# Optimization experiments

Measured on AMD Instinct MI355X. Metric: run time of the kernel, lower is better.

## Reference

```python
import jax, jax.numpy as jnp
import numpy as np

SMALL = 1e-7
EPS = 1e-6


def setup_inputs() -> dict:
    key = jax.random.key(0)
    k1, k2 = jax.random.split(key)
    B, C, h, w = 8, 3, 1024, 1024
    src = jax.random.normal(k1, (B, C, h, w), dtype=jnp.float32)
    # near-identity homographies so warped coords land mostly in-bounds
    H = jnp.eye(3, dtype=jnp.float32)[None] + 0.05 * jax.random.normal(k2, (B, 3, 3), dtype=jnp.float32)
    return {"src": src, "H": H}


def reference(src, H):
    B, C, h, w = src.shape
    # homogeneous pixel grid: (3, h, w) = [x, y, 1]
    xx = jnp.arange(w, dtype=jnp.float32)
    yy = jnp.arange(h, dtype=jnp.float32)
    gx, gy = jnp.meshgrid(xx, yy)  # (h, w) each
    grid = jnp.stack([gx, gy, jnp.ones_like(gx)], axis=0)  # (3, h, w)

    # per-pixel homography transform: (B,3,h,w)
    warped = jnp.einsum('bij,jhw->bihw', H, grid)
    T = warped[:, 2]  # (B,h,w)
    T = T + EPS * (1.0 - (jnp.abs(T) >= SMALL).astype(jnp.float32))
    x = warped[:, 0] / T  # (B,h,w) source x-coords
    y = warped[:, 1] / T  # (B,h,w) source y-coords

    # bilinear sample with clamped corner indices (matches torch impl)
    x0 = jnp.floor(x).astype(jnp.int32)
    y0 = jnp.floor(y).astype(jnp.int32)
    x1 = jnp.clip(x0 + 1, 0, w - 1)
    y1 = jnp.clip(y0 + 1, 0, h - 1)
    x0 = jnp.clip(x0, 0, w - 1)
    y0 = jnp.clip(y0, 0, h - 1)

    im = jnp.transpose(src, (0, 2, 3, 1))  # (B,h,w,C)
    b = jnp.arange(B, dtype=jnp.int32)[:, None, None]  # (B,1,1)
    Ia = im[b, y0, x0]  # (B,h,w,C)
    Ib = im[b, y1, x0]
    Ic = im[b, y0, x1]
    Id = im[b, y1, x1]

    x0f, x1f = x0.astype(jnp.float32), x1.astype(jnp.float32)
    y0f, y1f = y0.astype(jnp.float32), y1.astype(jnp.float32)
    wa = ((x1f - x) * (y1f - y))[..., None]
    wb = ((x1f - x) * (y - y0f))[..., None]
    wc = ((x - x0f) * (y1f - y))[..., None]
    wd = ((x - x0f) * (y - y0f))[..., None]

    out = wa * Ia + wb * Ib + wc * Ic + wd * Id  # (B,h,w,C)
    return jnp.transpose(out, (0, 3, 1, 2))  # (B,C,h,w)
```

## Files before the change

### kernel.cpp

```cpp
#include <hip/hip_runtime.h>
#include <math.h>
#include <limits.h>


#define SMALL_F 1e-7f
#define EPS_F   1e-6f

__device__ __forceinline__ int cvt_f32_i32_x86(float f) {
    if (f >= 2147483648.0f) return INT_MIN;
    return (int)f;
}

__global__ void __launch_bounds__(256)
warp_bilinear_kernel(const float* __restrict__ src, const float* __restrict__ Hm,
                     float* __restrict__ out, int B, int h, int w) {
#pragma clang fp contract(off)
    int x = blockIdx.x * blockDim.x + threadIdx.x;
    int y = blockIdx.y;
    int b = blockIdx.z;
    if (x >= w) return;

    const float* Hb = Hm + (size_t)b * 9;
    float gx = (float)x;
    float gy = (float)y;

    float w0 = (Hb[0] * gx + Hb[1] * gy) + Hb[2];
    float w1 = (Hb[3] * gx + Hb[4] * gy) + Hb[5];
    float T  = (Hb[6] * gx + Hb[7] * gy) + Hb[8];

    if (!(fabsf(T) >= SMALL_F)) T = T + EPS_F;

    float xs = w0 / T;
    float ys = w1 / T;

    float fx = floorf(xs);
    float fy = floorf(ys);
    int x0u = cvt_f32_i32_x86(fx);
    int y0u = cvt_f32_i32_x86(fy);

    int x1 = min(max(x0u + 1, 0), w - 1);
    int y1 = min(max(y0u + 1, 0), h - 1);
    int x0 = min(max(x0u, 0), w - 1);
    int y0 = min(max(y0u, 0), h - 1);

    float x0f = (float)x0, x1f = (float)x1;
    float y0f = (float)y0, y1f = (float)y1;

    float t1 = x1f - xs;
    float t2 = y1f - ys;
    float t3 = ys - y0f;
    float t4 = xs - x0f;

    float wa = t1 * t2;
    float wb = t1 * t3;
    float wc = t4 * t2;
    float wd = t4 * t3;

    const size_t plane = (size_t)h * (size_t)w;
    const float* sb = src + (size_t)b * 3u * plane;
    size_t i00 = (size_t)y0 * (size_t)w + (size_t)x0;
    size_t i10 = (size_t)y1 * (size_t)w + (size_t)x0;
    size_t i01 = (size_t)y0 * (size_t)w + (size_t)x1;
    size_t i11 = (size_t)y1 * (size_t)w + (size_t)x1;

    size_t o = (size_t)b * 3u * plane + (size_t)y * (size_t)w + (size_t)x;

#pragma unroll
    for (int c = 0; c < 3; ++c) {
        const float* sc = sb + (size_t)c * plane;
        float Ia = sc[i00];
        float Ib = sc[i10];
        float Ic = sc[i01];
        float Id = sc[i11];
        float r = ((wa * Ia + wb * Ib) + wc * Ic) + wd * Id;
        out[o + (size_t)c * plane] = r;
    }
}

extern "C" void kernel_launch(void* const* d_in, const int* in_sizes, int n_in,
                              void* d_out, int out_size, void* d_ws, size_t ws_size,
                              hipStream_t stream) {
    const float* src = (const float*)d_in[0];
    const float* Hm  = (const float*)d_in[1];
    float* out = (float*)d_out;

    const int B = in_sizes[1] / 9;
    const int C = 3;
    const size_t plane = (size_t)in_sizes[0] / ((size_t)B * C);
    const int h = 1024;
    const int w = (int)(plane / h);

    dim3 block(256, 1, 1);
    dim3 grid((w + 255) / 256, h, B);
    warp_bilinear_kernel<<<grid, block, 0, stream>>>(src, Hm, out, B, h, w);
}
```

Measured before the change: 224.8 us.

## Process four pixels per thread with paired 8-byte corner loads and nontemporal stores

Each thread now handles four output pixels strided by 256, hoisting the homography coefficients and row terms out of the per-pixel work. The two horizontally adjacent corners of each row are fetched with one 8-byte load from a clamped base column, and selects pick the right values at the borders. Outputs are written with nontemporal stores so they do not pollute cache that the gather reads rely on. The intent is fewer load instructions and less per-pixel overhead, at the cost of more registers per thread, four times fewer blocks, and possibly misaligned 8-byte loads.

```diff
diff --git a/kernel.cpp b/kernel.cpp
--- a/kernel.cpp
+++ b/kernel.cpp
@@ -1,10 +1,12 @@
 #include <hip/hip_runtime.h>
 #include <math.h>
 #include <limits.h>
+#include <string.h>
 
 
 #define SMALL_F 1e-7f
 #define EPS_F   1e-6f
+#define PX 4
 
 __device__ __forceinline__ int cvt_f32_i32_x86(float f) {
     if (f >= 2147483648.0f) return INT_MIN;
@@ -15,65 +17,76 @@
 warp_bilinear_kernel(const float* __restrict__ src, const float* __restrict__ Hm,
                      float* __restrict__ out, int B, int h, int w) {
 #pragma clang fp contract(off)
-    int x = blockIdx.x * blockDim.x + threadIdx.x;
-    int y = blockIdx.y;
-    int b = blockIdx.z;
-    if (x >= w) return;
+    const int y  = blockIdx.y;
+    const int b  = blockIdx.z;
+    const int tx = threadIdx.x;
+    const int xstart = blockIdx.x * (256 * PX) + tx;
 
     const float* Hb = Hm + (size_t)b * 9;
-    float gx = (float)x;
-    float gy = (float)y;
+    const float H0 = Hb[0], H1 = Hb[1], H2 = Hb[2];
+    const float H3 = Hb[3], H4 = Hb[4], H5 = Hb[5];
+    const float H6 = Hb[6], H7 = Hb[7], H8 = Hb[8];
+    const float gy = (float)y;
+    const float p1 = H1 * gy, p4 = H4 * gy, p7 = H7 * gy;
 
-    float w0 = (Hb[0] * gx + Hb[1] * gy) + Hb[2];
-    float w1 = (Hb[3] * gx + Hb[4] * gy) + Hb[5];
-    float T  = (Hb[6] * gx + Hb[7] * gy) + Hb[8];
+    int   idx0[PX], idx1[PX];
+    float wav[PX], wbv[PX], wcv[PX], wdv[PX];
+    bool  sA[PX], sC[PX], valid[PX];
 
-    if (!(fabsf(T) >= SMALL_F)) T = T + EPS_F;
-
-    float xs = w0 / T;
-    float ys = w1 / T;
-
-    float fx = floorf(xs);
-    float fy = floorf(ys);
-    int x0u = cvt_f32_i32_x86(fx);
-    int y0u = cvt_f32_i32_x86(fy);
-
-    int x1 = min(max(x0u + 1, 0), w - 1);
-    int y1 = min(max(y0u + 1, 0), h - 1);
-    int x0 = min(max(x0u, 0), w - 1);
-    int y0 = min(max(y0u, 0), h - 1);
-
-    float x0f = (float)x0, x1f = (float)x1;
-    float y0f = (float)y0, y1f = (float)y1;
-
-    float t1 = x1f - xs;
-    float t2 = y1f - ys;
-    float t3 = ys - y0f;
-    float t4 = xs - x0f;
-
-    float wa = t1 * t2;
-    float wb = t1 * t3;
-    float wc = t4 * t2;
-    float wd = t4 * t3;
+#pragma unroll
+    for (int k = 0; k < PX; ++k) {
+        int x = xstart + 256 * k;
+        valid[k] = (x < w);
+        float gx = (float)x;
+        float w0 = (H0 * gx + p1) + H2;
+        float w1 = (H3 * gx + p4) + H5;
+        float T  = (H6 * gx + p7) + H8;
+        if (!(fabsf(T) >= SMALL_F)) T = T + EPS_F;
+        float xs = w0 / T;
+        float ys = w1 / T;
+        float fx = floorf(xs), fy = floorf(ys);
+        int x0u = cvt_f32_i32_x86(fx);
+        int y0u = cvt_f32_i32_x86(fy);
+        int x1 = min(max(x0u + 1, 0), w - 1);
+        int y1 = min(max(y0u + 1, 0), h - 1);
+        int x0 = min(max(x0u, 0), w - 1);
+        int y0 = min(max(y0u, 0), h - 1);
+        float t1 = (float)x1 - xs;
+        float t2 = (float)y1 - ys;
+        float t3 = ys - (float)y0;
+        float t4 = xs - (float)x0;
+        wav[k] = t1 * t2;
+        wbv[k] = t1 * t3;
+        wcv[k] = t4 * t2;
+        wdv[k] = t4 * t3;
+        int xb = min(max(x0u, 0), w - 2);
+        sA[k] = (x0 == xb);
+        sC[k] = (x1 == xb);
+        idx0[k] = y0 * w + xb;
+        idx1[k] = y1 * w + xb;
+    }
 
     const size_t plane = (size_t)h * (size_t)w;
-    const float* sb = src + (size_t)b * 3u * plane;
-    size_t i00 = (size_t)y0 * (size_t)w + (size_t)x0;
-    size_t i10 = (size_t)y1 * (size_t)w + (size_t)x0;
-    size_t i01 = (size_t)y0 * (size_t)w + (size_t)x1;
-    size_t i11 = (size_t)y1 * (size_t)w + (size_t)x1;
-
-    size_t o = (size_t)b * 3u * plane + (size_t)y * (size_t)w + (size_t)x;
+    const float* sb = src + (size_t)b * 3 * plane;
+    float* ob = out + (size_t)b * 3 * plane + (size_t)y * (size_t)w;
 
 #pragma unroll
     for (int c = 0; c < 3; ++c) {
         const float* sc = sb + (size_t)c * plane;
-        float Ia = sc[i00];
-        float Ib = sc[i10];
-        float Ic = sc[i01];
-        float Id = sc[i11];
-        float r = ((wa * Ia + wb * Ib) + wc * Ic) + wd * Id;
-        out[o + (size_t)c * plane] = r;
+        float* oc = ob + (size_t)c * plane;
+#pragma unroll
+        for (int k = 0; k < PX; ++k) {
+            if (!valid[k]) continue;
+            float pr0[2], pr1[2];
+            __builtin_memcpy(pr0, sc + idx0[k], 8);
+            __builtin_memcpy(pr1, sc + idx1[k], 8);
+            float Ia = sA[k] ? pr0[0] : pr0[1];
+            float Ic = sC[k] ? pr0[0] : pr0[1];
+            float Ib = sA[k] ? pr1[0] : pr1[1];
+            float Id = sC[k] ? pr1[0] : pr1[1];
+            float r = ((wav[k] * Ia + wbv[k] * Ib) + wcv[k] * Ic) + wdv[k] * Id;
+            __builtin_nontemporal_store(r, oc + xstart + 256 * k);
+        }
     }
 }
 
@@ -91,6 +104,6 @@
     const int w = (int)(plane / h);
 
     dim3 block(256, 1, 1);
-    dim3 grid((w + 255) / 256, h, B);
+    dim3 grid((w + 256 * PX - 1) / (256 * PX), h, B);
     warp_bilinear_kernel<<<grid, block, 0, stream>>>(src, Hm, out, B, h, w);
 }
```

Result: faster. 186.0 us (-17.3%).
